# Optimization experiments

Hardware: AMD Instinct MI355X
Metric: run time of the kernel (lower is better)

Reference implementation:

```python
import jax, jax.numpy as jnp
import numpy as np

B, L, D = 2, 4096, 2048
H, K = 32, 16              # num_heads, mini_batch_size
HD = D // H                # head_dim = 64
NMB = L // K               # 256 mini-batches
TTT_BASE_LR = 1.0
LN_EPS = 1e-6


def setup_inputs() -> dict:
    key = jax.random.key(0)
    ks = jax.random.split(key, 16)
    r = lambda k, s: 0.02 * jax.random.normal(k, s, dtype=jnp.float32)
    return {
        "hidden_states": jax.random.normal(ks[0], (B, L, D), dtype=jnp.float32),
        "wq_w": r(ks[1], (D, D)), "wq_b": r(ks[2], (D,)),
        "wk_w": r(ks[3], (D, D)), "wk_b": r(ks[4], (D,)),
        "wv_w": r(ks[5], (D, D)), "wv_b": r(ks[6], (D,)),
        "wo_w": r(ks[7], (D, D)), "wo_b": r(ks[8], (D,)),
        "ttt_norm_weight": 1.0 + r(ks[9], (H, HD)),
        "ttt_norm_bias": r(ks[10], (H, HD)),
        "lr_w": r(ks[11], (H, 1, D)),       # learnable_ttt_lr_weight
        "lr_b": r(ks[12], (H, 1)),          # learnable_ttt_lr_bias
        "W1": r(ks[13], (H, HD, HD)),
        "b1": r(ks[14], (H, 1, HD)),
        "post_norm_w": jnp.ones((D,), jnp.float32),
        "post_norm_b": jnp.zeros((D,), jnp.float32),
    }


def ln_fwd(x, gamma, beta, eps=LN_EPS):
    mu = x.mean(-1, keepdims=True)
    var = ((x - mu) ** 2).mean(-1, keepdims=True)
    return gamma * ((x - mu) / jnp.sqrt(var + eps)) + beta


def ln_fused_l2_bwd(x, l2_target, gamma, beta, eps=LN_EPS):
    # grad of 0.5*||LN(x)*gamma+beta - target||^2 w.r.t. x (standard TTT helper)
    Dd = x.shape[-1]
    mu = x.mean(-1, keepdims=True)
    var = ((x - mu) ** 2).mean(-1, keepdims=True)
    std = jnp.sqrt(var + eps)
    x_hat = (x - mu) / std
    grad_x_hat = (gamma * x_hat + beta - l2_target) * gamma
    return (Dd * grad_x_hat
            - grad_x_hat.sum(-1, keepdims=True)
            - x_hat * (x_hat * grad_x_hat).sum(-1, keepdims=True)) / (Dd * std)


def reference(hidden_states, wq_w, wq_b, wk_w, wk_b, wv_w, wv_b, wo_w, wo_b,
              ttt_norm_weight, ttt_norm_bias, lr_w, lr_b, W1, b1,
              post_norm_w, post_norm_b):
    # QKV projections
    XQ = (hidden_states @ wq_w + wq_b).reshape(B, L, H, HD)
    XK = (hidden_states @ wk_w + wk_b).reshape(B, L, H, HD)
    XV = (hidden_states @ wv_w + wv_b).reshape(B, L, H, HD)
    # L2 normalize q/k per head (F.normalize, eps=1e-12)
    XQ = XQ / jnp.maximum(jnp.linalg.norm(XQ, axis=-1, keepdims=True), 1e-12)
    XK = XK / jnp.maximum(jnp.linalg.norm(XK, axis=-1, keepdims=True), 1e-12)
    # ln_reconstruction_target: torch.std is unbiased (ddof=1), eps added to std
    diff = XV - XK
    mu = diff.mean(-1, keepdims=True)
    std = jnp.std(diff, axis=-1, ddof=1, keepdims=True)
    XV = (ttt_norm_weight[None, None] * ((diff - mu) / (std + 1e-8))
          + ttt_norm_bias[None, None]) + XK
    # reshape to mini-batches: [B,H,NMB,K,HD]
    Xmb = hidden_states.reshape(B, NMB, K, D)
    tohd = lambda t: t.transpose(0, 2, 1, 3).reshape(B, H, NMB, K, HD)
    XQ, XK, XV = tohd(XQ), tohd(XK), tohd(XV)
    # eta gate: einsum('bnkc,hdc->bhnkd') with d==1, sigmoid, scale
    ttt_lr = jnp.einsum('bnkc,hdc->bhnkd', Xmb, lr_w) + lr_b.reshape(1, H, 1, 1, 1)
    ttt_lr = jax.nn.sigmoid(ttt_lr).transpose(0, 1, 2, 4, 3) * (TTT_BASE_LR / HD)  # [B,H,NMB,1,K]
    eta = jnp.broadcast_to(ttt_lr / K, (B, H, NMB, K, K))
    ln_w = ttt_norm_weight[:, None, :]  # [H,1,HD]
    ln_b = ttt_norm_bias[:, None, :]
    tril = jnp.tril(jnp.ones((K, K), jnp.float32))
    W1s = jnp.broadcast_to(W1[None], (B, H, HD, HD))
    b1s = jnp.broadcast_to(b1[None], (B, H, 1, HD))

    def step(carry, xs):
        W1c, b1c = carry
        xq, xk, xv, eta_mb = xs  # [B,H,K,HD], eta [B,H,K,K]
        Z1 = xk @ W1c + b1c
        grad = ln_fused_l2_bwd(Z1, xv - xk, ln_w, ln_b)        # [B,H,K,HD]
        Attn1 = tril * (xq @ xk.transpose(0, 1, 3, 2))         # causal within mini-batch
        b1_bar = b1c - (tril * eta_mb) @ grad
        Z1_bar = xq @ W1c - (eta_mb * Attn1) @ grad + b1_bar
        last_eta = eta_mb[:, :, -1, :, None]                   # [B,H,K,1]
        W1n = W1c - (last_eta * xk).transpose(0, 1, 3, 2) @ grad
        b1n = b1c - jnp.sum(last_eta * grad, axis=-2, keepdims=True)
        out = xq + ln_fwd(Z1_bar, ln_w, ln_b)
        return (W1n, b1n), out

    xs = tuple(t.transpose(2, 0, 1, 3, 4) for t in (XQ, XK, XV, eta))
    _, outs = jax.lax.scan(step, (W1s, b1s), xs)               # [NMB,B,H,K,HD]
    y = outs.transpose(1, 0, 3, 2, 4).reshape(B, L, D)
    # post_norm LayerNorm(eps=1e-6) then output projection
    mu = y.mean(-1, keepdims=True)
    var = ((y - mu) ** 2).mean(-1, keepdims=True)
    y = (y - mu) / jnp.sqrt(var + 1e-6) * post_norm_w + post_norm_b
    return y @ wo_w + wo_b
```

## Files before the change

kernel.cpp:

```cpp
#include <hip/hip_runtime.h>
#include <hip/hip_bf16.h>
#include <cstdint>
#include <cstddef>

#define DEV __device__ __forceinline__

constexpr int Bb = 2, Ls = 4096, Dd = 2048, Hh = 32, HD = 64, MBK = 16, NMBc = 256;
constexpr int MTOK = Bb * Ls;

typedef __bf16 bf16x8 __attribute__((ext_vector_type(8)));
typedef float  f32x4  __attribute__((ext_vector_type(4)));

DEV unsigned short f2bf(float f) {
    union { __bf16 h; unsigned short u; } x;
    x.h = (__bf16)f;
    return x.u;
}
DEV float b2f(unsigned short u) {
    union { unsigned int i; float f; } x; x.i = ((unsigned int)u) << 16;
    return x.f;
}

DEV void bsync() {
    asm volatile("s_waitcnt lgkmcnt(0)" ::: "memory");
    __builtin_amdgcn_s_barrier();
    asm volatile("" ::: "memory");
}

DEV float wsum64(float v) {
    int t;
    t = __builtin_amdgcn_update_dpp(0, __float_as_int(v), 0x111, 0xf, 0xf, true); v += __int_as_float(t);
    t = __builtin_amdgcn_update_dpp(0, __float_as_int(v), 0x112, 0xf, 0xf, true); v += __int_as_float(t);
    t = __builtin_amdgcn_update_dpp(0, __float_as_int(v), 0x114, 0xf, 0xf, true); v += __int_as_float(t);
    t = __builtin_amdgcn_update_dpp(0, __float_as_int(v), 0x118, 0xf, 0xf, true); v += __int_as_float(t);
    t = __builtin_amdgcn_update_dpp(0, __float_as_int(v), 0x142, 0xa, 0xf, true); v += __int_as_float(t);
    t = __builtin_amdgcn_update_dpp(0, __float_as_int(v), 0x143, 0xc, 0xf, true); v += __int_as_float(t);
    return __int_as_float(__builtin_amdgcn_readlane(__float_as_int(v), 63));
}

DEV float rsum16(float v) {
    int t;
    t = __builtin_amdgcn_update_dpp(0, __float_as_int(v), 0x121, 0xf, 0xf, true); v += __int_as_float(t);
    t = __builtin_amdgcn_update_dpp(0, __float_as_int(v), 0x122, 0xf, 0xf, true); v += __int_as_float(t);
    t = __builtin_amdgcn_update_dpp(0, __float_as_int(v), 0x124, 0xf, 0xf, true); v += __int_as_float(t);
    t = __builtin_amdgcn_update_dpp(0, __float_as_int(v), 0x128, 0xf, 0xf, true); v += __int_as_float(t);
    return v;
}

DEV float sel4(int n, float a, float b, float c, float d) {
    float v = (n == 1) ? b : a;
    v = (n == 2) ? c : v;
    v = (n == 3) ? d : v;
    return v;
}

DEV void g2l16(const void* g, void* l) {
    __builtin_amdgcn_global_load_lds(
        (__attribute__((address_space(1))) void*)(g),
        (__attribute__((address_space(3))) void*)(l), 16, 0, 0);
}

__global__ __launch_bounds__(256) void cast_hs_kernel(const float* __restrict__ src,
                                                      unsigned short* __restrict__ dst) {
    int i = (blockIdx.x * 256 + threadIdx.x) * 4;
    float4 v = *(const float4*)(src + i);
    ushort4 o; o.x = f2bf(v.x); o.y = f2bf(v.y); o.z = f2bf(v.z); o.w = f2bf(v.w);
    *(ushort4*)(dst + i) = o;
}

__global__ __launch_bounds__(256) void transpose_cast_kernel(const float* __restrict__ W,
                                                             unsigned short* __restrict__ Wt) {
    __shared__ float tile[64][65];
    int bx = blockIdx.x & 31;
    int by = blockIdx.x >> 5;
    int t = threadIdx.x;
    int r = t >> 4, c4 = (t & 15) * 4;
    #pragma unroll
    for (int i = 0; i < 4; ++i) {
        int row = r + i * 16;
        float4 v = *(const float4*)(W + (size_t)(bx * 64 + row) * Dd + by * 64 + c4);
        tile[row][c4 + 0] = v.x; tile[row][c4 + 1] = v.y;
        tile[row][c4 + 2] = v.z; tile[row][c4 + 3] = v.w;
    }
    __syncthreads();
    #pragma unroll
    for (int i = 0; i < 4; ++i) {
        int row = r + i * 16;
        ushort4 o;
        o.x = f2bf(tile[c4 + 0][row]); o.y = f2bf(tile[c4 + 1][row]);
        o.z = f2bf(tile[c4 + 2][row]); o.w = f2bf(tile[c4 + 3][row]);
        *(ushort4*)(Wt + (size_t)(by * 64 + row) * Dd + bx * 64 + c4) = o;
    }
}

__global__ __launch_bounds__(256) void gemm_bt_kernel(const unsigned short* __restrict__ A,
                                                      const unsigned short* __restrict__ Bt,
                                                      const float* __restrict__ bias,
                                                      float* __restrict__ C,
                                                      int M, int N, int Kd) {
    __shared__ unsigned short sA[128 * 64];
    __shared__ unsigned short sB[128 * 64];
    int t = threadIdx.x;
    int lane = t & 63;
    int wid = t >> 6, wm = wid >> 1, wn = wid & 1;
    int quad = lane >> 4, c = lane & 15;
    int bm = blockIdx.x, bn = blockIdx.y;

    const unsigned short* pa[4]; const unsigned short* pb[4];
    unsigned short* la[4]; unsigned short* lb[4];
    #pragma unroll
    for (int i = 0; i < 4; ++i) {
        int lin = i * 256 + t;
        int row = lin >> 3, blk = lin & 7;
        int oct = blk ^ (row & 7);
        pa[i] = A  + (size_t)(bm * 128 + row) * Kd + oct * 8;
        pb[i] = Bt + (size_t)(bn * 128 + row) * Kd + oct * 8;
        la[i] = sA + lin * 8;
        lb[i] = sB + lin * 8;
    }

    f32x4 acc[4][4];
    #pragma unroll
    for (int i = 0; i < 4; ++i)
        #pragma unroll
        for (int j = 0; j < 4; ++j)
            #pragma unroll
            for (int r = 0; r < 4; ++r) acc[i][j][r] = 0.f;

    const char* sAc = (const char*)sA;
    const char* sBc = (const char*)sB;
    int rowA0 = wm * 64 + c, rowB0 = wn * 64 + c;
    int sw = (c & 7);

    int nkt = Kd >> 6;
    for (int kt = 0; kt < nkt; ++kt) {
        #pragma unroll
        for (int i = 0; i < 4; ++i) {
            g2l16(pa[i], la[i]);
            g2l16(pb[i], lb[i]);
            pa[i] += 64; pb[i] += 64;
        }
        __syncthreads();
        #pragma unroll
        for (int s = 0; s < 2; ++s) {
            bf16x8 af[4], bfv[4];
            int so = (s << 2) | quad;
            #pragma unroll
            for (int mt = 0; mt < 4; ++mt)
                af[mt] = *(const bf16x8*)(sAc + (rowA0 + mt * 16) * 128 + ((so ^ sw) * 16));
            #pragma unroll
            for (int nt = 0; nt < 4; ++nt)
                bfv[nt] = *(const bf16x8*)(sBc + (rowB0 + nt * 16) * 128 + ((so ^ sw) * 16));
            #pragma unroll
            for (int mt = 0; mt < 4; ++mt)
                #pragma unroll
                for (int nt = 0; nt < 4; ++nt)
                    acc[mt][nt] = __builtin_amdgcn_mfma_f32_16x16x32_bf16(af[mt], bfv[nt], acc[mt][nt], 0, 0, 0);
        }
        __syncthreads();
    }

    float bv[4];
    #pragma unroll
    for (int nt = 0; nt < 4; ++nt) bv[nt] = bias[bn * 128 + wn * 64 + nt * 16 + c];
    #pragma unroll
    for (int mt = 0; mt < 4; ++mt)
        #pragma unroll
        for (int r = 0; r < 4; ++r) {
            int row = bm * 128 + wm * 64 + mt * 16 + quad * 4 + r;
            float* cp = C + (size_t)row * N + bn * 128 + wn * 64 + c;
            #pragma unroll
            for (int nt = 0; nt < 4; ++nt) cp[nt * 16] = acc[mt][nt][r] + bv[nt];
        }
}

__global__ __launch_bounds__(256) void lr_kernel(const float* __restrict__ hs,
                                                 const float* __restrict__ lrw,
                                                 const float* __restrict__ lrb,
                                                 float* __restrict__ lr_out) {
    int tok = blockIdx.x;
    int t = threadIdx.x;
    int h = t >> 3, j0 = t & 7;
    const float* row = hs + (size_t)tok * Dd;
    const float* wr = lrw + (size_t)h * Dd;
    float p = 0.f;
    for (int j = j0 * 4; j < Dd; j += 32) {
        float4 a = *(const float4*)(row + j);
        float4 w = *(const float4*)(wr + j);
        p += a.x * w.x + a.y * w.y + a.z * w.z + a.w * w.w;
    }
    __shared__ float red[32][8];
    red[h][j0] = p;
    __syncthreads();
    if (t < 32) {
        float s = 0.f;
        #pragma unroll
        for (int i = 0; i < 8; ++i) s += red[t][i];
        s += lrb[t];
        s = 1.f / (1.f + expf(-s));
        s *= 1.0f / (HD * MBK);
        int b = tok >> 12, l = tok & (Ls - 1);
        lr_out[(size_t)(b * Hh + t) * Ls + l] = s;
    }
}

DEV void stage_q_half(float4 q, float* tq, unsigned short* bq, int rowp, int c4p) {
    float rq = 1.f / fmaxf(sqrtf(rsum16(q.x*q.x + q.y*q.y + q.z*q.z + q.w*q.w)), 1e-12f);
    q.x *= rq; q.y *= rq; q.z *= rq; q.w *= rq;
    *(float4*)&tq[rowp * 68 + c4p] = q;
    ushort4 qb;
    qb.x = f2bf(q.x); qb.y = f2bf(q.y); qb.z = f2bf(q.z); qb.w = f2bf(q.w);
    *(ushort4*)&bq[rowp * 72 + c4p] = qb;
}
DEV void stage_kv_half(float4 k, float4 v, float* tk, float* tv, unsigned short* bk,
                       int rowp, int c4p, float4 lnw4, float4 lnb4) {
    float rk = 1.f / fmaxf(sqrtf(rsum16(k.x*k.x + k.y*k.y + k.z*k.z + k.w*k.w)), 1e-12f);
    k.x *= rk; k.y *= rk; k.z *= rk; k.w *= rk;
    float4 df; df.x = v.x - k.x; df.y = v.y - k.y; df.z = v.z - k.z; df.w = v.w - k.w;
    float mu = rsum16(df.x + df.y + df.z + df.w) * (1.f / 64.f);
    float4 cc; cc.x = df.x - mu; cc.y = df.y - mu; cc.z = df.z - mu; cc.w = df.w - mu;
    float var = rsum16(cc.x*cc.x + cc.y*cc.y + cc.z*cc.z + cc.w*cc.w) * (1.f / 63.f);
    float rs = 1.f / (sqrtf(var) + 1e-8f);
    float4 vn;
    vn.x = lnw4.x * cc.x * rs + lnb4.x + k.x;
    vn.y = lnw4.y * cc.y * rs + lnb4.y + k.y;
    vn.z = lnw4.z * cc.z * rs + lnb4.z + k.z;
    vn.w = lnw4.w * cc.w * rs + lnb4.w + k.w;
    *(float4*)&tk[rowp * 68 + c4p] = k;
    *(float4*)&tv[rowp * 68 + c4p] = vn;
    ushort4 kb;
    kb.x = f2bf(k.x); kb.y = f2bf(k.y); kb.z = f2bf(k.z); kb.w = f2bf(k.w);
    *(ushort4*)&bk[rowp * 72 + c4p] = kb;
}

__global__ __launch_bounds__(512, 1) void scan_kernel(const float* __restrict__ XQ,
                                                      const float* __restrict__ XK,
                                                      const float* __restrict__ XV,
                                                      const float* __restrict__ lrbuf,
                                                      const float* __restrict__ W1in,
                                                      const float* __restrict__ b1in,
                                                      const float* __restrict__ lnw_g,
                                                      const float* __restrict__ lnb_g,
                                                      float* __restrict__ Y) {
    int bh = blockIdx.x;
    int b = bh >> 5, h = bh & 31;
    int t = threadIdx.x;
    int w = t >> 6;
    int lane = t & 63;
    int q = lane >> 4, n = lane & 15;
    int role = w >> 2, wz = w & 3;
    int gc = 16 * wz + n;

    __shared__ float tiles[2][3][16 * 68];
    __shared__ unsigned short tbq[2][16 * 72];
    __shared__ unsigned short tbk[2][16 * 72];
    __shared__ float svb[2][16];
    __shared__ unsigned short wt_hi[64 * 72];
    __shared__ unsigned short wt_lo[64 * 72];
    __shared__ float zTr[16 * 68];
    __shared__ unsigned short gbufT[64 * 32];
    __shared__ unsigned short sxkT[64 * 32];
    __shared__ unsigned short attb[2][16 * 32];
    __shared__ float pb[8 * 64];
    __shared__ float s1p[16 * 4], s2p[16 * 4];
    __shared__ float s1z[16 * 4], s2z[16 * 4];

    #pragma unroll
    for (int i = 0; i < 8; ++i) {
        int k = i * 8 + w;
        float val = W1in[(size_t)h * 4096 + (size_t)k * 64 + lane];
        unsigned short hi = f2bf(val);
        unsigned short lo = f2bf(val - b2f(hi));
        wt_hi[lane * 72 + k] = hi;
        wt_lo[lane * 72 + k] = lo;
    }
    #pragma unroll
    for (int i = 0; i < 4; ++i) { gbufT[i * 512 + t] = 0; sxkT[i * 512 + t] = 0; }
    #pragma unroll
    for (int i = 0; i < 2; ++i) ((unsigned short*)attb)[i * 512 + t] = 0;

    float b1r = b1in[h * 64 + lane];
    float b1c = b1in[h * 64 + gc];
    float lnwr = lnw_g[h * 64 + lane];
    float lnbr = lnb_g[h * 64 + lane];
    float lnwc = lnw_g[h * 64 + gc];
    float lnbc = lnb_g[h * 64 + gc];

    const size_t gbase = ((size_t)b * Ls) * Dd + h * 64;
    const float* lrp = lrbuf + (size_t)bh * Ls;

    int ts = t & 255;
    int rowp = ts >> 4, c4p = (ts & 15) * 4;
    float4 lnw4 = *(const float4*)(lnw_g + h * 64 + c4p);
    float4 lnb4 = *(const float4*)(lnb_g + h * 64 + c4p);

    float4 preq, prek, prev;
    if (role == 0) {
        float4 q0 = *(const float4*)(XQ + gbase + (size_t)rowp * Dd + c4p);
        stage_q_half(q0, &tiles[0][0][0], tbq[0], rowp, c4p);
        preq = *(const float4*)(XQ + gbase + (size_t)(16 + rowp) * Dd + c4p);
    } else {
        float4 k0 = *(const float4*)(XK + gbase + (size_t)rowp * Dd + c4p);
        float4 v0 = *(const float4*)(XV + gbase + (size_t)rowp * Dd + c4p);
        stage_kv_half(k0, v0, &tiles[0][1][0], &tiles[0][2][0], tbk[0], rowp, c4p, lnw4, lnb4);
        prek = *(const float4*)(XK + gbase + (size_t)(16 + rowp) * Dd + c4p);
        prev = *(const float4*)(XV + gbase + (size_t)(16 + rowp) * Dd + c4p);
    }
    if (t < 16) svb[0][t] = lrp[t];
    float presv = (t < 16) ? lrp[16 + t] : 0.f;
    bsync();

    const f32x4 zero4 = {0.f, 0.f, 0.f, 0.f};
    float zbar_p[4] = {0.f, 0.f, 0.f, 0.f};
    float xqc_p[4]  = {0.f, 0.f, 0.f, 0.f};

    for (int nmb = 0; nmb < NMBc; ++nmb) {
        int cb = nmb & 1, nb2 = cb ^ 1;
        int l0 = nmb * 16;
        int lp = (l0 + 32 <= Ls - 16) ? (l0 + 32) : (Ls - 16);
        if (role == 0) {
            stage_q_half(preq, &tiles[nb2][0][0], tbq[nb2], rowp, c4p);
            preq = *(const float4*)(XQ + gbase + (size_t)(lp + rowp) * Dd + c4p);
        } else {
            stage_kv_half(prek, prev, &tiles[nb2][1][0], &tiles[nb2][2][0], tbk[nb2],
                          rowp, c4p, lnw4, lnb4);
            prek = *(const float4*)(XK + gbase + (size_t)(lp + rowp) * Dd + c4p);
            prev = *(const float4*)(XV + gbase + (size_t)(lp + rowp) * Dd + c4p);
        }
        if (t < 16) svb[nb2][t] = presv;
        presv = (t < 16) ? lrp[lp + t] : 0.f;

        const float* xqs = &tiles[cb][0][0];
        const float* xks = &tiles[cb][1][0];
        const float* xvs = &tiles[cb][2][0];
        const unsigned short* bqs = tbq[cb];
        const unsigned short* bks = tbk[cb];

        bf16x8 wh0 = *(const bf16x8*)&wt_hi[gc * 72 + 8 * q];
        bf16x8 wh1 = *(const bf16x8*)&wt_hi[gc * 72 + 32 + 8 * q];
        bf16x8 wl0 = *(const bf16x8*)&wt_lo[gc * 72 + 8 * q];
        bf16x8 wl1 = *(const bf16x8*)&wt_lo[gc * 72 + 32 + 8 * q];

        f32x4 zb = zero4;
        if (role == 0) {
            bf16x8 kf0 = *(const bf16x8*)&bks[n * 72 + 8 * q];
            bf16x8 kf1 = *(const bf16x8*)&bks[n * 72 + 32 + 8 * q];
            f32x4 z1 = __builtin_amdgcn_mfma_f32_16x16x32_bf16(kf0, wh0, zero4, 0, 0, 0);
            z1 = __builtin_amdgcn_mfma_f32_16x16x32_bf16(kf1, wh1, z1, 0, 0, 0);
            f32x4 z1l = __builtin_amdgcn_mfma_f32_16x16x32_bf16(kf0, wl0, zero4, 0, 0, 0);
            z1l = __builtin_amdgcn_mfma_f32_16x16x32_bf16(kf1, wl1, z1l, 0, 0, 0);
            z1 = z1 + z1l;
            float p1[4], p2[4];
            #pragma unroll
            for (int r = 0; r < 4; ++r) {
                zTr[(4 * q + r) * 68 + gc] = z1[r];
                float za = z1[r] + b1c;
                p1[r] = rsum16(za);
                p2[r] = rsum16(za * za);
            }
            if (n < 4) {
                s1p[(4 * q + n) * 4 + wz] = sel4(n, p1[0], p1[1], p1[2], p1[3]);
                s2p[(4 * q + n) * 4 + wz] = sel4(n, p2[0], p2[1], p2[2], p2[3]);
            }
        } else {
            bf16x8 qf0 = *(const bf16x8*)&bqs[n * 72 + 8 * q];
            bf16x8 qf1 = *(const bf16x8*)&bqs[n * 72 + 32 + 8 * q];
            zb = __builtin_amdgcn_mfma_f32_16x16x32_bf16(qf0, wh0, zero4, 0, 0, 0);
            zb = __builtin_amdgcn_mfma_f32_16x16x32_bf16(qf1, wh1, zb, 0, 0, 0);
            f32x4 zbl = __builtin_amdgcn_mfma_f32_16x16x32_bf16(qf0, wl0, zero4, 0, 0, 0);
            zbl = __builtin_amdgcn_mfma_f32_16x16x32_bf16(qf1, wl1, zbl, 0, 0, 0);
            zb = zb + zbl;
            if (w == 4) {
                bf16x8 kf0 = *(const bf16x8*)&bks[n * 72 + 8 * q];
                bf16x8 kf1 = *(const bf16x8*)&bks[n * 72 + 32 + 8 * q];
                f32x4 aacc = __builtin_amdgcn_mfma_f32_16x16x32_bf16(qf1, kf1, zero4, 0, 0, 0);
                aacc = __builtin_amdgcn_mfma_f32_16x16x32_bf16(qf0, kf0, aacc, 0, 0, 0);
                float svn = svb[cb][n];
                #pragma unroll
                for (int r = 0; r < 4; ++r) {
                    int i = 4 * q + r;
                    attb[cb][i * 32 + n] = f2bf((i >= n) ? (-svn * (aacc[r] + 1.f)) : 0.f);
                }
            }
        }
        bsync();

        if (role == 1 && nmb > 0) {
            int l0p = l0 - 16;
            #pragma unroll
            for (int r = 0; r < 4; ++r) {
                int row = 4 * q + r;
                float4 a1 = *(const float4*)&s1z[row * 4];
                float4 a2 = *(const float4*)&s2z[row * 4];
                float s1 = a1.x + a1.y + a1.z + a1.w;
                float s2 = a2.x + a2.y + a2.z + a2.w;
                float mu = s1 * (1.f / 64.f);
                float var = s2 * (1.f / 64.f) - mu * mu;
                float rstd = rsqrtf(var + 1e-6f);
                float o = lnwc * ((zbar_p[r] - mu) * rstd) + lnbc + xqc_p[r];
                Y[gbase + (size_t)(l0p + row) * Dd + gc] = o;
            }
        }

        float zar[2], xk_rm[2], xv_rm[2];
        #pragma unroll
        for (int r = 0; r < 2; ++r) {
            int rw = 2 * w + r;
            zar[r] = zTr[rw * 68 + lane] + b1r;
            xk_rm[r] = xks[rw * 68 + lane];
            xv_rm[r] = xvs[rw * 68 + lane];
        }
        float svr[2] = { svb[cb][2 * w], svb[cb][2 * w + 1] };
        float gr[2]; float pbv = 0.f;
        #pragma unroll
        for (int r = 0; r < 2; ++r) {
            int rw = 2 * w + r;
            float4 a1 = *(const float4*)&s1p[rw * 4];
            float4 a2 = *(const float4*)&s2p[rw * 4];
            float s1 = a1.x + a1.y + a1.z + a1.w;
            float s2 = a2.x + a2.y + a2.z + a2.w;
            float mu = s1 * (1.f / 64.f);
            float var = s2 * (1.f / 64.f) - mu * mu;
            float rstd = rsqrtf(var + 1e-6f);
            float xh = (zar[r] - mu) * rstd;
            float g = (lnwr * xh + lnbr - (xv_rm[r] - xk_rm[r])) * lnwr;
            float sg = wsum64(g);
            float sxg = wsum64(xh * g);
            gr[r] = (64.f * g - sg - xh * sxg) * rstd * (1.f / 64.f);
            pbv += svr[r] * gr[r];
        }
        {
            ushort2 gp, sp;
            gp.x = f2bf(gr[0]); gp.y = f2bf(gr[1]);
            sp.x = f2bf(svr[0] * xk_rm[0]); sp.y = f2bf(svr[1] * xk_rm[1]);
            *(ushort2*)&gbufT[lane * 32 + 2 * w] = gp;
            *(ushort2*)&sxkT[lane * 32 + 2 * w] = sp;
            pb[w * 64 + lane] = pbv;
        }
        bsync();

        bf16x8 gF = *(const bf16x8*)&gbufT[gc * 32 + 8 * q];
        if (role == 0) {
            #pragma unroll
            for (int tm = 0; tm < 4; ++tm) {
                bf16x8 ax = *(const bf16x8*)&sxkT[(16 * tm + n) * 32 + 8 * q];
                f32x4 dl = __builtin_amdgcn_mfma_f32_16x16x32_bf16(ax, gF, zero4, 0, 0, 0);
                int ko = 16 * tm + 4 * q;
                ushort4 h4 = *(ushort4*)&wt_hi[gc * 72 + ko];
                ushort4 l4 = *(ushort4*)&wt_lo[gc * 72 + ko];
                float w0 = b2f(h4.x) + b2f(l4.x) - dl[0];
                float w1 = b2f(h4.y) + b2f(l4.y) - dl[1];
                float w2 = b2f(h4.z) + b2f(l4.z) - dl[2];
                float w3 = b2f(h4.w) + b2f(l4.w) - dl[3];
                h4.x = f2bf(w0); l4.x = f2bf(w0 - b2f(h4.x));
                h4.y = f2bf(w1); l4.y = f2bf(w1 - b2f(h4.y));
                h4.z = f2bf(w2); l4.z = f2bf(w2 - b2f(h4.z));
                h4.w = f2bf(w3); l4.w = f2bf(w3 - b2f(h4.w));
                *(ushort4*)&wt_hi[gc * 72 + ko] = h4;
                *(ushort4*)&wt_lo[gc * 72 + ko] = l4;
            }
        } else {
            bf16x8 amF = *(const bf16x8*)&attb[cb][n * 32 + 8 * q];
            zb = __builtin_amdgcn_mfma_f32_16x16x32_bf16(amF, gF, zb, 0, 0, 0);
            float pz1[4], pz2[4];
            #pragma unroll
            for (int r = 0; r < 4; ++r) {
                zbar_p[r] = zb[r] + b1c;
                pz1[r] = rsum16(zbar_p[r]);
                pz2[r] = rsum16(zbar_p[r] * zbar_p[r]);
                xqc_p[r] = xqs[(4 * q + r) * 68 + gc];
            }
            if (n < 4) {
                s1z[(4 * q + n) * 4 + wz] = sel4(n, pz1[0], pz1[1], pz1[2], pz1[3]);
                s2z[(4 * q + n) * 4 + wz] = sel4(n, pz2[0], pz2[1], pz2[2], pz2[3]);
            }
        }
        {
            float sbr = 0.f, sbc = 0.f;
            #pragma unroll
            for (int i = 0; i < 8; ++i) { sbr += pb[i * 64 + lane]; sbc += pb[i * 64 + gc]; }
            b1r -= sbr; b1c -= sbc;
        }
        bsync();
    }

    if (role == 1) {
        int l0p = (NMBc - 1) * 16;
        #pragma unroll
        for (int r = 0; r < 4; ++r) {
            int row = 4 * q + r;
            float4 a1 = *(const float4*)&s1z[row * 4];
            float4 a2 = *(const float4*)&s2z[row * 4];
            float s1 = a1.x + a1.y + a1.z + a1.w;
            float s2 = a2.x + a2.y + a2.z + a2.w;
            float mu = s1 * (1.f / 64.f);
            float var = s2 * (1.f / 64.f) - mu * mu;
            float rstd = rsqrtf(var + 1e-6f);
            float o = lnwc * ((zbar_p[r] - mu) * rstd) + lnbc + xqc_p[r];
            Y[gbase + (size_t)(l0p + row) * Dd + gc] = o;
        }
    }
}

__global__ __launch_bounds__(256) void postnorm_kernel(const float* __restrict__ Y,
                                                       const float* __restrict__ pw,
                                                       const float* __restrict__ pb,
                                                       unsigned short* __restrict__ Yb) {
    int tok = blockIdx.x, t = threadIdx.x;
    const float* row = Y + (size_t)tok * Dd;
    int c0 = t * 4, c1 = 1024 + t * 4;
    float4 v0 = *(const float4*)(row + c0);
    float4 v1 = *(const float4*)(row + c1);
    float s1 = v0.x + v0.y + v0.z + v0.w + v1.x + v1.y + v1.z + v1.w;
    float s2 = v0.x * v0.x + v0.y * v0.y + v0.z * v0.z + v0.w * v0.w +
               v1.x * v1.x + v1.y * v1.y + v1.z * v1.z + v1.w * v1.w;
    s1 = wsum64(s1); s2 = wsum64(s2);
    __shared__ float r1[4], r2[4];
    if ((t & 63) == 0) { r1[t >> 6] = s1; r2[t >> 6] = s2; }
    __syncthreads();
    float S1 = r1[0] + r1[1] + r1[2] + r1[3];
    float S2 = r2[0] + r2[1] + r2[2] + r2[3];
    float mu = S1 * (1.f / 2048.f);
    float var = S2 * (1.f / 2048.f) - mu * mu;
    float rstd = rsqrtf(var + 1e-6f);
    float4 w0 = *(const float4*)(pw + c0), b0 = *(const float4*)(pb + c0);
    float4 w1 = *(const float4*)(pw + c1), b1 = *(const float4*)(pb + c1);
    ushort4 o0, o1;
    o0.x = f2bf((v0.x - mu) * rstd * w0.x + b0.x);
    o0.y = f2bf((v0.y - mu) * rstd * w0.y + b0.y);
    o0.z = f2bf((v0.z - mu) * rstd * w0.z + b0.z);
    o0.w = f2bf((v0.w - mu) * rstd * w0.w + b0.w);
    o1.x = f2bf((v1.x - mu) * rstd * w1.x + b1.x);
    o1.y = f2bf((v1.y - mu) * rstd * w1.y + b1.y);
    o1.z = f2bf((v1.z - mu) * rstd * w1.z + b1.z);
    o1.w = f2bf((v1.w - mu) * rstd * w1.w + b1.w);
    *(ushort4*)(Yb + (size_t)tok * Dd + c0) = o0;
    *(ushort4*)(Yb + (size_t)tok * Dd + c1) = o1;
}

extern "C" void kernel_launch(void* const* d_in, const int* in_sizes, int n_in,
                              void* d_out, int out_size, void* d_ws, size_t ws_size,
                              hipStream_t stream) {
    const float* hs   = (const float*)d_in[0];
    const float* wq_w = (const float*)d_in[1];
    const float* wq_b = (const float*)d_in[2];
    const float* wk_w = (const float*)d_in[3];
    const float* wk_b = (const float*)d_in[4];
    const float* wv_w = (const float*)d_in[5];
    const float* wv_b = (const float*)d_in[6];
    const float* wo_w = (const float*)d_in[7];
    const float* wo_b = (const float*)d_in[8];
    const float* lnw  = (const float*)d_in[9];
    const float* lnb  = (const float*)d_in[10];
    const float* lr_w = (const float*)d_in[11];
    const float* lr_b = (const float*)d_in[12];
    const float* W1   = (const float*)d_in[13];
    const float* b1   = (const float*)d_in[14];
    const float* pnw  = (const float*)d_in[15];
    const float* pnb  = (const float*)d_in[16];
    float* out = (float*)d_out;

    char* ws = (char*)d_ws;
    size_t off = 0;
    auto alloc = [&](size_t bytes) -> void* {
        void* p = ws + off; off += (bytes + 255) & ~(size_t)255; return p;
    };
    unsigned short* hsb = (unsigned short*)alloc((size_t)MTOK * Dd * 2);
    unsigned short* wtb = (unsigned short*)alloc((size_t)Dd * Dd * 2);
    float* XQ = (float*)alloc((size_t)MTOK * Dd * 4);
    float* XK = (float*)alloc((size_t)MTOK * Dd * 4);
    float* XV = (float*)alloc((size_t)MTOK * Dd * 4);
    float* lrbuf = (float*)alloc((size_t)Bb * Hh * Ls * 4);
    float* Y = XQ;
    unsigned short* Yb = hsb;

    dim3 blk(256);
    cast_hs_kernel<<<dim3(MTOK * Dd / 1024), blk, 0, stream>>>(hs, hsb);

    transpose_cast_kernel<<<dim3(1024), blk, 0, stream>>>(wq_w, wtb);
    gemm_bt_kernel<<<dim3(64, 16), blk, 0, stream>>>(hsb, wtb, wq_b, XQ, MTOK, Dd, Dd);
    transpose_cast_kernel<<<dim3(1024), blk, 0, stream>>>(wk_w, wtb);
    gemm_bt_kernel<<<dim3(64, 16), blk, 0, stream>>>(hsb, wtb, wk_b, XK, MTOK, Dd, Dd);
    transpose_cast_kernel<<<dim3(1024), blk, 0, stream>>>(wv_w, wtb);
    gemm_bt_kernel<<<dim3(64, 16), blk, 0, stream>>>(hsb, wtb, wv_b, XV, MTOK, Dd, Dd);

    lr_kernel<<<dim3(MTOK), blk, 0, stream>>>(hs, lr_w, lr_b, lrbuf);

    scan_kernel<<<dim3(Bb * Hh), dim3(512), 0, stream>>>(XQ, XK, XV, lrbuf, W1, b1, lnw, lnb, Y);

    postnorm_kernel<<<dim3(MTOK), blk, 0, stream>>>(Y, pnw, pnb, Yb);

    transpose_cast_kernel<<<dim3(1024), blk, 0, stream>>>(wo_w, wtb);
    gemm_bt_kernel<<<dim3(64, 16), blk, 0, stream>>>(Yb, wtb, wo_b, out, MTOK, Dd, Dd);
}
```

Baseline: 1.401 ms.

## Replace GEMM with 256x256 double-buffered pipelined kernel with block swizzle

Replaces the 128x128 single-buffered bf16 MFMA GEMM with a 256x256-tile, 512-thread kernel. It double-buffers LDS and interleaves global-to-LDS staging of the next tiles with MFMA work across four phases, using fine-grained barriers, vmcnt waits and setprio. It also adds a block-index swizzle for L2 locality. The larger tiles cut global traffic per FLOP and the pipelining hides load latency, at the cost of more registers and 128KB of LDS per block, which limits occupancy.

```diff
diff --git a/kernel.cpp b/kernel.cpp
--- a/kernel.cpp
+++ b/kernel.cpp
@@ -93,84 +93,128 @@
     }
 }
 
-__global__ __launch_bounds__(256) void gemm_bt_kernel(const unsigned short* __restrict__ A,
-                                                      const unsigned short* __restrict__ Bt,
-                                                      const float* __restrict__ bias,
-                                                      float* __restrict__ C,
-                                                      int M, int N, int Kd) {
-    __shared__ unsigned short sA[128 * 64];
-    __shared__ unsigned short sB[128 * 64];
+__global__ __launch_bounds__(512, 2) void gemm256_kernel(const unsigned short* __restrict__ A,
+                                                         const unsigned short* __restrict__ Bt,
+                                                         const float* __restrict__ bias,
+                                                         float* __restrict__ C,
+                                                         int M, int N, int Kd) {
+    __shared__ unsigned short sA[2][256 * 64];
+    __shared__ unsigned short sB[2][256 * 64];
     int t = threadIdx.x;
     int lane = t & 63;
-    int wid = t >> 6, wm = wid >> 1, wn = wid & 1;
-    int quad = lane >> 4, c = lane & 15;
-    int bm = blockIdx.x, bn = blockIdx.y;
-
-    const unsigned short* pa[4]; const unsigned short* pb[4];
-    unsigned short* la[4]; unsigned short* lb[4];
-    #pragma unroll
-    for (int i = 0; i < 4; ++i) {
-        int lin = i * 256 + t;
-        int row = lin >> 3, blk = lin & 7;
-        int oct = blk ^ (row & 7);
-        pa[i] = A  + (size_t)(bm * 128 + row) * Kd + oct * 8;
-        pb[i] = Bt + (size_t)(bn * 128 + row) * Kd + oct * 8;
-        la[i] = sA + lin * 8;
-        lb[i] = sB + lin * 8;
-    }
-
-    f32x4 acc[4][4];
-    #pragma unroll
-    for (int i = 0; i < 4; ++i)
+    int wid = t >> 6;
+    int wm = wid >> 2, wn = wid & 3;
+    int q = lane >> 4, n = lane & 15;
+
+    int cpx = gridDim.x >> 3;
+    int swz = (blockIdx.x & 7) * cpx + (blockIdx.x >> 3);
+    int nbn = N >> 8;
+    int bm = swz / nbn, bn = swz % nbn;
+
+    int r0 = t >> 3;
+    int kc = (t & 7) ^ (r0 & 7);
+    int lo0 = t * 8;
+    const unsigned short* gA = A + (size_t)(bm * 256) * Kd;
+    const unsigned short* gB = Bt + (size_t)(bn * 256) * Kd;
+
+    auto stageA = [&](int buf, int half, int kt) {
+        const unsigned short* s0 = gA + (size_t)(half * 128 + r0) * Kd + kt * 64 + kc * 8;
+        const unsigned short* s1 = gA + (size_t)(half * 128 + 64 + r0) * Kd + kt * 64 + kc * 8;
+        g2l16(s0, &sA[buf][half * 8192 + lo0]);
+        g2l16(s1, &sA[buf][half * 8192 + 4096 + lo0]);
+    };
+    auto stageB = [&](int buf, int half, int kt) {
+        const unsigned short* s0 = gB + (size_t)(half * 128 + r0) * Kd + kt * 64 + kc * 8;
+        const unsigned short* s1 = gB + (size_t)(half * 128 + 64 + r0) * Kd + kt * 64 + kc * 8;
+        g2l16(s0, &sB[buf][half * 8192 + lo0]);
+        g2l16(s1, &sB[buf][half * 8192 + 4096 + lo0]);
+    };
+
+    f32x4 acc[8][4];
+    #pragma unroll
+    for (int i = 0; i < 8; ++i)
         #pragma unroll
         for (int j = 0; j < 4; ++j)
             #pragma unroll
             for (int r = 0; r < 4; ++r) acc[i][j][r] = 0.f;
 
-    const char* sAc = (const char*)sA;
-    const char* sBc = (const char*)sB;
-    int rowA0 = wm * 64 + c, rowB0 = wn * 64 + c;
-    int sw = (c & 7);
-
     int nkt = Kd >> 6;
-    for (int kt = 0; kt < nkt; ++kt) {
+
+    stageA(0, 0, 0); stageA(0, 1, 0);
+    stageB(0, 0, 0); stageB(0, 1, 0);
+    stageB(1, 0, 1); stageB(1, 1, 1);
+    asm volatile("s_waitcnt vmcnt(4)" ::: "memory");
+    __builtin_amdgcn_s_barrier();
+    asm volatile("" ::: "memory");
+
+    for (int G = 0; G < nkt; ++G) {
+        int cur = G & 1;
+        const unsigned short* bA = sA[cur];
+        const unsigned short* bB = sB[cur];
+        bf16x8 bfv[4][2];
         #pragma unroll
-        for (int i = 0; i < 4; ++i) {
-            g2l16(pa[i], la[i]);
-            g2l16(pb[i], lb[i]);
-            pa[i] += 64; pb[i] += 64;
-        }
-        __syncthreads();
-        #pragma unroll
-        for (int s = 0; s < 2; ++s) {
-            bf16x8 af[4], bfv[4];
-            int so = (s << 2) | quad;
-            #pragma unroll
-            for (int mt = 0; mt < 4; ++mt)
-                af[mt] = *(const bf16x8*)(sAc + (rowA0 + mt * 16) * 128 + ((so ^ sw) * 16));
-            #pragma unroll
-            for (int nt = 0; nt < 4; ++nt)
-                bfv[nt] = *(const bf16x8*)(sBc + (rowB0 + nt * 16) * 128 + ((so ^ sw) * 16));
-            #pragma unroll
-            for (int mt = 0; mt < 4; ++mt)
+        for (int p = 0; p < 4; ++p) {
+            bf16x8 af[2][2];
+            #pragma unroll
+            for (int mi = 0; mi < 2; ++mi) {
+                int row = wm * 128 + (2 * p + mi) * 16 + n;
+                #pragma unroll
+                for (int kk = 0; kk < 2; ++kk)
+                    af[mi][kk] = *(const bf16x8*)&bA[row * 64 + (((kk * 4 + q) ^ (n & 7)) * 8)];
+            }
+            if (p == 0) {
+                #pragma unroll
+                for (int nt = 0; nt < 4; ++nt) {
+                    int row = wn * 64 + nt * 16 + n;
+                    #pragma unroll
+                    for (int kk = 0; kk < 2; ++kk)
+                        bfv[nt][kk] = *(const bf16x8*)&bB[row * 64 + (((kk * 4 + q) ^ (n & 7)) * 8)];
+                }
+            }
+            if (p == 0) { if (G + 1 < nkt) stageA(cur ^ 1, 0, G + 1); }
+            if (p == 1) { if (G + 1 < nkt) stageA(cur ^ 1, 1, G + 1); }
+            if (p == 2) { if (G + 2 < nkt) stageB(cur, 0, G + 2); }
+            if (p == 3) { if (G + 2 < nkt) stageB(cur, 1, G + 2); }
+
+            asm volatile("" ::: "memory");
+            __builtin_amdgcn_s_barrier();
+            asm volatile("s_waitcnt lgkmcnt(0)" ::: "memory");
+            __builtin_amdgcn_sched_barrier(0);
+            __builtin_amdgcn_s_setprio(1);
+            #pragma unroll
+            for (int mi = 0; mi < 2; ++mi)
                 #pragma unroll
                 for (int nt = 0; nt < 4; ++nt)
-                    acc[mt][nt] = __builtin_amdgcn_mfma_f32_16x16x32_bf16(af[mt], bfv[nt], acc[mt][nt], 0, 0, 0);
-        }
-        __syncthreads();
+                    acc[2 * p + mi][nt] = __builtin_amdgcn_mfma_f32_16x16x32_bf16(
+                        af[mi][0], bfv[nt][0], acc[2 * p + mi][nt], 0, 0, 0);
+            #pragma unroll
+            for (int mi = 0; mi < 2; ++mi)
+                #pragma unroll
+                for (int nt = 0; nt < 4; ++nt)
+                    acc[2 * p + mi][nt] = __builtin_amdgcn_mfma_f32_16x16x32_bf16(
+                        af[mi][1], bfv[nt][1], acc[2 * p + mi][nt], 0, 0, 0);
+            __builtin_amdgcn_s_setprio(0);
+            if (p == 3) {
+                if (G + 2 >= nkt) asm volatile("s_waitcnt vmcnt(0)" ::: "memory");
+                else              asm volatile("s_waitcnt vmcnt(4)" ::: "memory");
+            }
+            asm volatile("" ::: "memory");
+            __builtin_amdgcn_s_barrier();
+            asm volatile("" ::: "memory");
+        }
     }
 
     float bv[4];
     #pragma unroll
-    for (int nt = 0; nt < 4; ++nt) bv[nt] = bias[bn * 128 + wn * 64 + nt * 16 + c];
-    #pragma unroll
-    for (int mt = 0; mt < 4; ++mt)
+    for (int nt = 0; nt < 4; ++nt) bv[nt] = bias[bn * 256 + wn * 64 + nt * 16 + n];
+    #pragma unroll
+    for (int m = 0; m < 8; ++m)
         #pragma unroll
         for (int r = 0; r < 4; ++r) {
-            int row = bm * 128 + wm * 64 + mt * 16 + quad * 4 + r;
-            float* cp = C + (size_t)row * N + bn * 128 + wn * 64 + c;
-            #pragma unroll
-            for (int nt = 0; nt < 4; ++nt) cp[nt * 16] = acc[mt][nt][r] + bv[nt];
+            int row = bm * 256 + wm * 128 + m * 16 + 4 * q + r;
+            float* cp = C + (size_t)row * N + bn * 256 + wn * 64 + n;
+            #pragma unroll
+            for (int nt = 0; nt < 4; ++nt) cp[nt * 16] = acc[m][nt][r] + bv[nt];
         }
 }
 
@@ -575,14 +619,17 @@
     unsigned short* Yb = hsb;
 
     dim3 blk(256);
+    dim3 gblk(512);
+    dim3 ggrid((MTOK / 256) * (Dd / 256));
+
     cast_hs_kernel<<<dim3(MTOK * Dd / 1024), blk, 0, stream>>>(hs, hsb);
 
     transpose_cast_kernel<<<dim3(1024), blk, 0, stream>>>(wq_w, wtb);
-    gemm_bt_kernel<<<dim3(64, 16), blk, 0, stream>>>(hsb, wtb, wq_b, XQ, MTOK, Dd, Dd);
+    gemm256_kernel<<<ggrid, gblk, 0, stream>>>(hsb, wtb, wq_b, XQ, MTOK, Dd, Dd);
     transpose_cast_kernel<<<dim3(1024), blk, 0, stream>>>(wk_w, wtb);
-    gemm_bt_kernel<<<dim3(64, 16), blk, 0, stream>>>(hsb, wtb, wk_b, XK, MTOK, Dd, Dd);
+    gemm256_kernel<<<ggrid, gblk, 0, stream>>>(hsb, wtb, wk_b, XK, MTOK, Dd, Dd);
     transpose_cast_kernel<<<dim3(1024), blk, 0, stream>>>(wv_w, wtb);
-    gemm_bt_kernel<<<dim3(64, 16), blk, 0, stream>>>(hsb, wtb, wv_b, XV, MTOK, Dd, Dd);
+    gemm256_kernel<<<ggrid, gblk, 0, stream>>>(hsb, wtb, wv_b, XV, MTOK, Dd, Dd);
 
     lr_kernel<<<dim3(MTOK), blk, 0, stream>>>(hs, lr_w, lr_b, lrbuf);
 
@@ -591,5 +638,5 @@
     postnorm_kernel<<<dim3(MTOK), blk, 0, stream>>>(Y, pnw, pnb, Yb);
 
     transpose_cast_kernel<<<dim3(1024), blk, 0, stream>>>(wo_w, wtb);
-    gemm_bt_kernel<<<dim3(64, 16), blk, 0, stream>>>(Yb, wtb, wo_b, out, MTOK, Dd, Dd);
-}
+    gemm256_kernel<<<ggrid, gblk, 0, stream>>>(Yb, wtb, wo_b, out, MTOK, Dd, Dd);
+}
```

Result: faster. 1.320 ms (-5.8%).
